# Performance work log

Hardware: AMD Instinct MI355X
Metric: run time of the kernel (lower is better)

Reference implementation:

```python
import jax, jax.numpy as jnp
import numpy as np

B, S, D = 2, 2048, 1024
H = 16
HS = D // H  # head_size = 64
SCALE = HS ** 0.5


def setup_inputs() -> dict:
    key = jax.random.key(0)
    ks = jax.random.split(key, 7)
    std = 1.0 / np.sqrt(D)
    return {
        "x": jax.random.normal(ks[0], (B, S, D), dtype=jnp.float32),
        "Wq": jax.random.normal(ks[1], (D, D), dtype=jnp.float32) * std,
        "bq": jax.random.normal(ks[2], (D,), dtype=jnp.float32) * std,
        "Wk": jax.random.normal(ks[3], (D, D), dtype=jnp.float32) * std,
        "bk": jax.random.normal(ks[4], (D,), dtype=jnp.float32) * std,
        "Wv": jax.random.normal(ks[5], (D, D), dtype=jnp.float32) * std,
        "bv": jax.random.normal(ks[6], (D,), dtype=jnp.float32) * std,
    }


def reference(x, Wq, bq, Wk, bk, Wv, bv):
    bs, seq, _ = x.shape
    # QKV projections (torch Linear: x @ W.T + b)
    Q = (x @ Wq.T + bq).reshape(bs, seq, H, HS)
    K = (x @ Wk.T + bk).reshape(bs, seq, H, HS)
    V = (x @ Wv.T + bv).reshape(bs, seq, H, HS)
    # scores[b,h,q,k] = Q . K / scale
    scores = jnp.einsum("bqhd,bkhd->bhqk", Q, K) / SCALE
    # causal mask: disallow k > q
    causal = jnp.triu(jnp.ones((seq, seq), dtype=bool), k=1)
    scores = jnp.where(causal, -jnp.inf, scores)
    probs = jax.nn.softmax(scores, axis=-1)
    att = jnp.einsum("bhqk,bkhd->bqhd", probs, V)
    return att.reshape(bs, seq, H * HS)
```

## Files before the change

### kernel.cpp

```cpp
#include <hip/hip_runtime.h>

typedef unsigned short ushort_t;
typedef __bf16 bf16x8 __attribute__((ext_vector_type(8)));
typedef unsigned short ushortx8 __attribute__((ext_vector_type(8)));
typedef unsigned short ushortx4 __attribute__((ext_vector_type(4)));
typedef unsigned int uintx4 __attribute__((ext_vector_type(4)));
typedef float floatx4 __attribute__((ext_vector_type(4)));
typedef float floatx16 __attribute__((ext_vector_type(16)));

__device__ inline void load16_lds(const ushort_t* g, ushort_t* l) {
  __builtin_amdgcn_global_load_lds(
      (__attribute__((address_space(1))) void*)(g),
      (__attribute__((address_space(3))) void*)(l),
      16, 0, 0);
}

__device__ inline float bf2f(ushort_t u) {
  unsigned int v = ((unsigned int)u) << 16;
  return __builtin_bit_cast(float, v);
}

__device__ inline ushort_t f2bf(float f) {
  unsigned int u = __builtin_bit_cast(unsigned int, f);
  u += 0x7fffu + ((u >> 16) & 1u);
  return (ushort_t)(u >> 16);
}

__device__ inline bf16x8 ldfrag(const ushort_t* p) {
  return __builtin_bit_cast(bf16x8, *(const ushortx8*)p);
}

__device__ inline unsigned cvtpk_bf16(float lo, float hi) {
  unsigned r;
  asm("v_cvt_pk_bf16_f32 %0, %1, %2" : "=v"(r) : "v"(lo), "v"(hi));
  return r;
}

__device__ inline void plswap(unsigned& a, unsigned& b) {
  asm("v_permlane32_swap_b32 %0, %1" : "+v"(a), "+v"(b));
}

__device__ inline bool sniff_f32(const ushort_t* x, int lane_off) {
  float v = fabsf(bf2f(x[lane_off]));
  bool big = !(v < 1e4f);
  return __ballot(big) != 0ull;
}

__global__ __launch_bounds__(256) void convert_all(
    const void* __restrict__ x,
    const void* __restrict__ wq, const void* __restrict__ wk, const void* __restrict__ wv,
    const void* __restrict__ bq, const void* __restrict__ bk, const void* __restrict__ bv,
    ushort_t* __restrict__ xb, ushort_t* __restrict__ wqb,
    ushort_t* __restrict__ wkb, ushort_t* __restrict__ wvb,
    float* __restrict__ biasf, int* __restrict__ flag)
{
  const bool f32 = sniff_f32((const ushort_t*)x, (int)(threadIdx.x & 63));
  const int seg = blockIdx.y;
  if (seg == 4) {
    if (blockIdx.x == 0 && threadIdx.x == 0) *flag = f32 ? 1 : 0;
    const int i = blockIdx.x * 256 + threadIdx.x;
    if (i >= 1024) return;
    const void* bs[3] = {bq, bk, bv};
#pragma unroll
    for (int k = 0; k < 3; ++k)
      biasf[k * 1024 + i] = f32 ? ((const float*)bs[k])[i] : bf2f(((const ushort_t*)bs[k])[i]);
    return;
  }
  const void* src = (seg == 0) ? x : (seg == 1) ? wq : (seg == 2) ? wk : wv;
  ushort_t* dst   = (seg == 0) ? xb : (seg == 1) ? wqb : (seg == 2) ? wkb : wvb;
  const int n = (seg == 0) ? 4194304 : 1048576;
  const int i = (blockIdx.x * 256 + threadIdx.x) * 8;
  if (i >= n) return;
  if (f32) {
    const float* s = (const float*)src + i;
    ushortx8 o;
#pragma unroll
    for (int j = 0; j < 8; ++j) o[j] = f2bf(s[j]);
    *(ushortx8*)(dst + i) = o;
  } else {
    *(ushortx8*)(dst + i) = *(const ushortx8*)((const ushort_t*)src + i);
  }
}

__global__ __launch_bounds__(256, 2) void qkv_gemm(
    const ushort_t* __restrict__ x,
    const ushort_t* __restrict__ Wq, const ushort_t* __restrict__ Wk,
    const ushort_t* __restrict__ Wv, const float* __restrict__ biasf,
    ushort_t* __restrict__ Qo, ushort_t* __restrict__ Ko, ushort_t* __restrict__ Vt)
{
  __shared__ __attribute__((aligned(16))) ushort_t As[128 * 32];
  __shared__ __attribute__((aligned(16))) ushort_t Bs[128 * 32];

  const int which = blockIdx.z;
  const ushort_t* W = (which == 0) ? Wq : (which == 1) ? Wk : Wv;
  const float oscale = (which == 0) ? 0.18033688011112042f : 1.0f;

  const int n0 = blockIdx.x * 128;
  const int m0 = blockIdx.y * 128;

  const int tid  = threadIdx.x;
  const int wave = tid >> 6;
  const int lane = tid & 63;
  const int ln   = lane & 15;
  const int quad = lane >> 4;
  const int wm = (wave >> 1) * 64;
  const int wn = (wave & 1) * 64;

  floatx4 acc[4][4];
#pragma unroll
  for (int i = 0; i < 4; ++i)
#pragma unroll
    for (int j = 0; j < 4; ++j) acc[i][j] = floatx4{0.f, 0.f, 0.f, 0.f};

  const int c1 = tid, c2 = tid + 256;
  const ushort_t* ga1 = x + (m0 + (c1 >> 2)) * 1024 + (c1 & 3) * 8;
  const ushort_t* ga2 = x + (m0 + (c2 >> 2)) * 1024 + (c2 & 3) * 8;
  const ushort_t* gb1 = W + (n0 + (c1 >> 2)) * 1024 + (c1 & 3) * 8;
  const ushort_t* gb2 = W + (n0 + (c2 >> 2)) * 1024 + (c2 & 3) * 8;
  ushort_t* la1 = As + wave * 512;
  ushort_t* la2 = As + 2048 + wave * 512;
  ushort_t* lb1 = Bs + wave * 512;
  ushort_t* lb2 = Bs + 2048 + wave * 512;

  for (int kt = 0; kt < 1024; kt += 32) {
    __syncthreads();
    load16_lds(ga1 + kt, la1);
    load16_lds(ga2 + kt, la2);
    load16_lds(gb1 + kt, lb1);
    load16_lds(gb2 + kt, lb2);
    __syncthreads();

    bf16x8 af[4], bfr[4];
#pragma unroll
    for (int mi = 0; mi < 4; ++mi)
      af[mi] = ldfrag(As + (wm + mi * 16 + ln) * 32 + quad * 8);
#pragma unroll
    for (int ni = 0; ni < 4; ++ni)
      bfr[ni] = ldfrag(Bs + (wn + ni * 16 + ln) * 32 + quad * 8);
#pragma unroll
    for (int mi = 0; mi < 4; ++mi)
#pragma unroll
      for (int ni = 0; ni < 4; ++ni)
        acc[mi][ni] = __builtin_amdgcn_mfma_f32_16x16x32_bf16(af[mi], bfr[ni], acc[mi][ni], 0, 0, 0);
  }

  float bvv[4];
#pragma unroll
  for (int ni = 0; ni < 4; ++ni) bvv[ni] = biasf[which * 1024 + n0 + wn + ni * 16 + ln];

  if (which == 2) {
#pragma unroll
    for (int mi = 0; mi < 4; ++mi)
#pragma unroll
      for (int ni = 0; ni < 4; ++ni) {
        const int col = n0 + wn + ni * 16 + ln;
        const int row0 = m0 + wm + mi * 16 + quad * 4;
        const int b = row0 >> 11, s0 = row0 & 2047;
        const int h = col >> 6, hs = col & 63;
        ushortx4 pk;
#pragma unroll
        for (int r = 0; r < 4; ++r) pk[r] = f2bf(acc[mi][ni][r] + bvv[ni]);
        *(ushortx4*)(Vt + ((size_t)((b * 16 + h) * 64 + hs)) * 2048 + s0) = pk;
      }
  } else {
    ushort_t* out = (which == 0) ? Qo : Ko;
#pragma unroll
    for (int mi = 0; mi < 4; ++mi)
#pragma unroll
      for (int ni = 0; ni < 4; ++ni) {
        const int col = n0 + wn + ni * 16 + ln;
#pragma unroll
        for (int r = 0; r < 4; ++r) {
          const int row = m0 + wm + mi * 16 + quad * 4 + r;
          out[row * 1024 + col] = f2bf((acc[mi][ni][r] + bvv[ni]) * oscale);
        }
      }
  }
}

__global__ __launch_bounds__(256) void flash20(
    const ushort_t* __restrict__ Q, const ushort_t* __restrict__ Kx,
    const ushort_t* __restrict__ Vt, void* __restrict__ out,
    const int* __restrict__ flag)
{
  __shared__ __attribute__((aligned(16))) ushort_t Kl[2][4096];
  __shared__ __attribute__((aligned(16))) ushort_t Vl[2][4096];

  const bool f32o = (*flag != 0);
  const int tid  = threadIdx.x;
  const int wave = tid >> 6;
  const int lane = tid & 63;
  const int l31 = lane & 31;
  const int hi  = lane >> 5;
  const int qsub = wave & 1;
  const int kvh  = wave >> 1;

#define CROW(r) (((r) & 3) + 8 * ((r) >> 2) + 4 * hi)

  const int i = blockIdx.x;
  const int xcd = i & 7, j = i >> 3;
  const int bh = xcd * 4 + (j & 3);
  const int cc = 31 - (j >> 2);
  const int b = bh >> 4, h = bh & 15;
  const int qblk = cc * 64;
  const int qw = qblk + 32 * qsub;
  const int nt = cc + 1;

  const ushort_t* kbase = Kx + ((size_t)b * 2048) * 1024 + h * 64;
  const ushort_t* vbase = Vt + (size_t)bh * 64 * 2048;

  const int srow = 8 * wave + (lane >> 3);
  const int sus  = (lane & 7) ^ (lane >> 3);
  const ushort_t* kp = kbase + (size_t)srow * 1024 + sus * 8;
  const ushort_t* vp = vbase + (size_t)srow * 2048 + sus * 8;

#define STAGE(BUFI, KV0) do {                                                 \
    const ushort_t* kp_ = kp + (size_t)(KV0) * 1024;                          \
    const ushort_t* vp_ = vp + (KV0);                                         \
    load16_lds(kp_,                     &Kl[BUFI][(wave << 6) * 8]);          \
    load16_lds(kp_ + 32 * 1024,         &Kl[BUFI][2048 + (wave << 6) * 8]);   \
    load16_lds(vp_,                     &Vl[BUFI][(wave << 6) * 8]);          \
    load16_lds(vp_ + (size_t)32 * 2048, &Vl[BUFI][2048 + (wave << 6) * 8]);   \
  } while (0)

  bf16x8 qf[4];
#pragma unroll
  for (int s = 0; s < 4; ++s)
    qf[s] = ldfrag(Q + (size_t)(b * 2048 + qw + l31) * 1024 + h * 64 + s * 16 + hi * 8);

  floatx16 ot[2];
#pragma unroll
  for (int dq = 0; dq < 2; ++dq)
#pragma unroll
    for (int r = 0; r < 16; ++r) ot[dq][r] = 0.f;
  float li = 0.f;

  const int swz = l31 & 7;

#define PACK_PV(BUFI, PARR, SH, KSTEP) do {                                   \
    unsigned X_ = cvtpk_bf16(PARR[8 * (SH) + 0], PARR[8 * (SH) + 1]);         \
    unsigned Y_ = cvtpk_bf16(PARR[8 * (SH) + 2], PARR[8 * (SH) + 3]);         \
    unsigned Z_ = cvtpk_bf16(PARR[8 * (SH) + 4], PARR[8 * (SH) + 5]);         \
    unsigned W_ = cvtpk_bf16(PARR[8 * (SH) + 6], PARR[8 * (SH) + 7]);         \
    plswap(X_, Z_);                                                           \
    plswap(Y_, W_);                                                           \
    uintx4 u_ = {X_, Y_, Z_, W_};                                             \
    const bf16x8 pa_ = __builtin_bit_cast(bf16x8, u_);                        \
    const bf16x8 v0_ = ldfrag(&Vl[BUFI][(l31) * 64 + ((2 * (KSTEP) + hi) ^ swz) * 8]);        \
    const bf16x8 v1_ = ldfrag(&Vl[BUFI][(32 + l31) * 64 + ((2 * (KSTEP) + hi) ^ swz) * 8]);   \
    ot[0] = __builtin_amdgcn_mfma_f32_32x32x16_bf16(pa_, v0_, ot[0], 0, 0, 0);\
    ot[1] = __builtin_amdgcn_mfma_f32_32x32x16_bf16(pa_, v1_, ot[1], 0, 0, 0);\
  } while (0)

#define COMPUTE(BUFI, KV0) do {                                               \
    const int krow_ = 32 * kvh + l31;                                         \
    bf16x8 kf0_ = ldfrag(&Kl[BUFI][krow_ * 64 + ((0 + hi) ^ swz) * 8]);       \
    bf16x8 kf1_ = ldfrag(&Kl[BUFI][krow_ * 64 + ((2 + hi) ^ swz) * 8]);       \
    bf16x8 kf2_ = ldfrag(&Kl[BUFI][krow_ * 64 + ((4 + hi) ^ swz) * 8]);       \
    bf16x8 kf3_ = ldfrag(&Kl[BUFI][krow_ * 64 + ((6 + hi) ^ swz) * 8]);       \
    floatx16 st_;                                                             \
    _Pragma("unroll")                                                         \
    for (int r = 0; r < 16; ++r) st_[r] = 0.f;                                \
    st_ = __builtin_amdgcn_mfma_f32_32x32x16_bf16(kf0_, qf[0], st_, 0, 0, 0); \
    st_ = __builtin_amdgcn_mfma_f32_32x32x16_bf16(kf1_, qf[1], st_, 0, 0, 0); \
    st_ = __builtin_amdgcn_mfma_f32_32x32x16_bf16(kf2_, qf[2], st_, 0, 0, 0); \
    st_ = __builtin_amdgcn_mfma_f32_32x32x16_bf16(kf3_, qf[3], st_, 0, 0, 0); \
    const int kvb_ = (KV0) + 32 * kvh;                                        \
    float p_[16];                                                             \
    if (kvb_ + 31 > qw) {                                                     \
      const int qg_ = qw + l31;                                               \
      _Pragma("unroll")                                                       \
      for (int r = 0; r < 16; ++r) {                                          \
        const int kva_ = kvb_ + CROW(r);                                      \
        const float e_ = __builtin_amdgcn_exp2f(st_[r]);                      \
        p_[r] = (kva_ > qg_) ? 0.f : e_;                                      \
      }                                                                       \
    } else {                                                                  \
      _Pragma("unroll")                                                       \
      for (int r = 0; r < 16; ++r) p_[r] = __builtin_amdgcn_exp2f(st_[r]);    \
    }                                                                         \
    float ls_ = 0.f;                                                          \
    _Pragma("unroll")                                                         \
    for (int r = 0; r < 16; ++r) ls_ += p_[r];                                \
    li += ls_;                                                                \
    PACK_PV(BUFI, p_, 0, 2 * kvh + 0);                                        \
    PACK_PV(BUFI, p_, 1, 2 * kvh + 1);                                        \
  } while (0)

  int cur = 0;
  STAGE(0, 0);
  if (nt > 1) STAGE(1, 64);
  for (int t = 0; t < nt; ++t) {
    if (t == nt - 1) {
      asm volatile("s_waitcnt vmcnt(0)" ::: "memory");
    } else {
      asm volatile("s_waitcnt vmcnt(4)" ::: "memory");
    }
    __builtin_amdgcn_sched_barrier(0);
    __builtin_amdgcn_s_barrier();

    const int kv0 = t * 64;
    if (kv0 + 32 * kvh <= qw + 31) COMPUTE(cur, kv0);

    asm volatile("s_waitcnt lgkmcnt(0)" ::: "memory");
    __builtin_amdgcn_sched_barrier(0);
    __builtin_amdgcn_s_barrier();

    if (t + 2 < nt) STAGE(cur, (t + 2) * 64);
    cur ^= 1;
  }

#undef STAGE
#undef PACK_PV
#undef COMPUTE

  float lf = li + __shfl_xor(li, 32);

  float* Sc = (float*)&Kl[0][0];
  float* Lc = (float*)&Vl[0][0];
  if (kvh == 1) {
#pragma unroll
    for (int dq = 0; dq < 2; ++dq)
#pragma unroll
      for (int r = 0; r < 16; ++r)
        Sc[qsub * 2048 + CROW(r) * 64 + 32 * dq + l31] = ot[dq][r];
    Lc[qsub * 32 + l31] = lf;
  }
  __syncthreads();
  if (kvh == 0) {
#pragma unroll
    for (int dq = 0; dq < 2; ++dq)
#pragma unroll
      for (int r = 0; r < 16; ++r)
        ot[dq][r] += Sc[qsub * 2048 + CROW(r) * 64 + 32 * dq + l31];
    lf += Lc[qsub * 32 + l31];
    Lc[64 + qsub * 32 + l31] = 1.0f / lf;

#pragma unroll
    for (int r = 0; r < 16; ++r) {
      const int q_ = qw + CROW(r);
      const float iv = Lc[64 + qsub * 32 + CROW(r)];
      if (f32o) {
        float* of = (float*)out;
#pragma unroll
        for (int dq = 0; dq < 2; ++dq)
          of[(size_t)(b * 2048 + q_) * 1024 + h * 64 + 32 * dq + l31] = ot[dq][r] * iv;
      } else {
        ushort_t* ob = (ushort_t*)out;
#pragma unroll
        for (int dq = 0; dq < 2; ++dq)
          ob[(size_t)(b * 2048 + q_) * 1024 + h * 64 + 32 * dq + l31] = f2bf(ot[dq][r] * iv);
      }
    }
  }
#undef CROW
}

extern "C" void kernel_launch(void* const* d_in, const int* in_sizes, int n_in,
                              void* d_out, int out_size, void* d_ws, size_t ws_size,
                              hipStream_t stream) {
  char* w = (char*)d_ws;
  int* flag = (int*)w;
  size_t off = 256;
  ushort_t* xb  = (ushort_t*)(w + off); off += (size_t)4194304 * 2;
  ushort_t* wqb = (ushort_t*)(w + off); off += (size_t)1048576 * 2;
  ushort_t* wkb = (ushort_t*)(w + off); off += (size_t)1048576 * 2;
  ushort_t* wvb = (ushort_t*)(w + off); off += (size_t)1048576 * 2;
  float* biasf  = (float*)(w + off);    off += (size_t)3 * 1024 * 4;
  ushort_t* Qw  = (ushort_t*)(w + off); off += (size_t)4194304 * 2;
  ushort_t* Kw  = (ushort_t*)(w + off); off += (size_t)4194304 * 2;
  ushort_t* Vtw = (ushort_t*)(w + off);

  convert_all<<<dim3(2048, 5), 256, 0, stream>>>(
      d_in[0], d_in[1], d_in[3], d_in[5], d_in[2], d_in[4], d_in[6],
      xb, wqb, wkb, wvb, biasf, flag);
  qkv_gemm<<<dim3(8, 32, 3), 256, 0, stream>>>(xb, wqb, wkb, wvb, biasf, Qw, Kw, Vtw);
  flash20<<<1024, 256, 0, stream>>>(Qw, Kw, Vtw, d_out, flag);
}
```

Before: 151.3 us.

## Double QKV GEMM K-tile to 64 with XOR-swizzled LDS layout

```diff
diff --git a/kernel.cpp b/kernel.cpp
--- a/kernel.cpp
+++ b/kernel.cpp
@@ -82,14 +82,14 @@
   }
 }
 
-__global__ __launch_bounds__(256, 2) void qkv_gemm(
+__global__ __launch_bounds__(256, 3) void qkv_gemm(
     const ushort_t* __restrict__ x,
     const ushort_t* __restrict__ Wq, const ushort_t* __restrict__ Wk,
     const ushort_t* __restrict__ Wv, const float* __restrict__ biasf,
     ushort_t* __restrict__ Qo, ushort_t* __restrict__ Ko, ushort_t* __restrict__ Vt)
 {
-  __shared__ __attribute__((aligned(16))) ushort_t As[128 * 32];
-  __shared__ __attribute__((aligned(16))) ushort_t Bs[128 * 32];
+  __shared__ __attribute__((aligned(16))) ushort_t As[128 * 64];
+  __shared__ __attribute__((aligned(16))) ushort_t Bs[128 * 64];
 
   const int which = blockIdx.z;
   const ushort_t* W = (which == 0) ? Wq : (which == 1) ? Wk : Wv;
@@ -112,36 +112,39 @@
 #pragma unroll
     for (int j = 0; j < 4; ++j) acc[i][j] = floatx4{0.f, 0.f, 0.f, 0.f};
 
-  const int c1 = tid, c2 = tid + 256;
-  const ushort_t* ga1 = x + (m0 + (c1 >> 2)) * 1024 + (c1 & 3) * 8;
-  const ushort_t* ga2 = x + (m0 + (c2 >> 2)) * 1024 + (c2 & 3) * 8;
-  const ushort_t* gb1 = W + (n0 + (c1 >> 2)) * 1024 + (c1 & 3) * 8;
-  const ushort_t* gb2 = W + (n0 + (c2 >> 2)) * 1024 + (c2 & 3) * 8;
-  ushort_t* la1 = As + wave * 512;
-  ushort_t* la2 = As + 2048 + wave * 512;
-  ushort_t* lb1 = Bs + wave * 512;
-  ushort_t* lb2 = Bs + 2048 + wave * 512;
-
-  for (int kt = 0; kt < 1024; kt += 32) {
+  const int r0 = tid >> 3;
+  const int su = (tid & 7) ^ (r0 & 7);
+  const ushort_t* ga = x + (size_t)(m0 + r0) * 1024 + su * 8;
+  const ushort_t* gb = W + (size_t)(n0 + r0) * 1024 + su * 8;
+
+  for (int kt = 0; kt < 1024; kt += 64) {
     __syncthreads();
-    load16_lds(ga1 + kt, la1);
-    load16_lds(ga2 + kt, la2);
-    load16_lds(gb1 + kt, lb1);
-    load16_lds(gb2 + kt, lb2);
+#pragma unroll
+    for (int i = 0; i < 4; ++i) {
+      load16_lds(ga + (size_t)(32 * i) * 1024 + kt, As + (i * 256 + tid) * 8);
+      load16_lds(gb + (size_t)(32 * i) * 1024 + kt, Bs + (i * 256 + tid) * 8);
+    }
     __syncthreads();
 
-    bf16x8 af[4], bfr[4];
-#pragma unroll
-    for (int mi = 0; mi < 4; ++mi)
-      af[mi] = ldfrag(As + (wm + mi * 16 + ln) * 32 + quad * 8);
-#pragma unroll
-    for (int ni = 0; ni < 4; ++ni)
-      bfr[ni] = ldfrag(Bs + (wn + ni * 16 + ln) * 32 + quad * 8);
-#pragma unroll
-    for (int mi = 0; mi < 4; ++mi)
-#pragma unroll
-      for (int ni = 0; ni < 4; ++ni)
-        acc[mi][ni] = __builtin_amdgcn_mfma_f32_16x16x32_bf16(af[mi], bfr[ni], acc[mi][ni], 0, 0, 0);
+#pragma unroll
+    for (int ks = 0; ks < 2; ++ks) {
+      bf16x8 af[4], bfr[4];
+#pragma unroll
+      for (int mi = 0; mi < 4; ++mi) {
+        const int row = wm + mi * 16 + ln;
+        af[mi] = ldfrag(As + row * 64 + (((ks << 2) + quad) ^ (row & 7)) * 8);
+      }
+#pragma unroll
+      for (int ni = 0; ni < 4; ++ni) {
+        const int row = wn + ni * 16 + ln;
+        bfr[ni] = ldfrag(Bs + row * 64 + (((ks << 2) + quad) ^ (row & 7)) * 8);
+      }
+#pragma unroll
+      for (int mi = 0; mi < 4; ++mi)
+#pragma unroll
+        for (int ni = 0; ni < 4; ++ni)
+          acc[mi][ni] = __builtin_amdgcn_mfma_f32_16x16x32_bf16(af[mi], bfr[ni], acc[mi][ni], 0, 0, 0);
+    }
   }
 
   float bvv[4];
```

New measurement: 148.6 us. Within noise of the previous version (-1.8%).
